# Optimization experiments

Hardware: AMD Instinct MI355X
Metric: run time of the kernel (lower is better)

## Reference

```python
import jax, jax.numpy as jnp
import numpy as np

NUM_EMBEDDINGS = 256
EMBEDDING_DIM = 8


def setup_inputs() -> dict:
    key = jax.random.key(0)
    ks = jax.random.split(key, 8)
    B, D_in, H, D_out = 1024, 512, 2048, 512
    s = lambda fan: 1.0 / np.sqrt(fan)
    return {
        "x": jax.random.normal(ks[0], (B, D_in), dtype=jnp.float32),
        "emb_W": jax.random.normal(ks[1], (NUM_EMBEDDINGS, EMBEDDING_DIM), dtype=jnp.float32),
        "W_in": jax.random.normal(ks[2], (H, D_in), dtype=jnp.float32) * s(D_in),
        "b_in": jax.random.normal(ks[3], (H,), dtype=jnp.float32) * s(D_in),
        "W_h": jax.random.normal(ks[4], (H, H), dtype=jnp.float32) * s(H),
        "b_h": jax.random.normal(ks[5], (H,), dtype=jnp.float32) * s(H),
        "W_out": jax.random.normal(ks[6], (D_out, H), dtype=jnp.float32) * s(H),
        "b_out": jax.random.normal(ks[7], (D_out,), dtype=jnp.float32) * s(H),
    }


def reference(x, emb_W, W_in, b_in, W_h, b_h, W_out, b_out):
    B, D_in = x.shape
    flat = x.reshape(-1)  # [B*D_in], row-major flatten == torch .flatten()
    # power-feature expansion: powers 1..embedding_dim stacked on axis 1
    exps = jnp.arange(1, EMBEDDING_DIM + 1, dtype=x.dtype)
    x_res = flat[:, None] ** exps[None, :]  # [B*D_in, E]
    # get_ind: NOTE source uses sum(flat_x) (not sum of squares) -- faithful
    sm = jnp.sum(x_res, axis=1, keepdims=True)              # [N,1]
    emb = jnp.sum(emb_W * emb_W, axis=1)[None, :]           # [1,K]
    dist = sm + emb - 2.0 * (x_res @ emb_W.T)               # [N,K]
    ind = jnp.argmin(dist, axis=1)                          # [N] int
    # q = ind.view_as(x.T).T : reshape to [D_in, B] then transpose
    q = ind.reshape(D_in, B).T.astype(x.dtype)              # [B, D_in]
    # straight-through: forward value q, gradient flows to x
    q = x + jax.lax.stop_gradient(q - x)
    relu = jax.nn.relu
    h = relu(q @ W_in.T + b_in)      # d_in
    for _ in range(4):               # shared d_h applied 4 times
        h = relu(h @ W_h.T + b_h)
    f = relu(h @ W_out.T + b_out)    # d_out
    q_latent_loss = jnp.float32(0.0)  # eval mode
    return (f, q_latent_loss)
```

## Files before the change

### kernel.cpp

```cpp
#include <hip/hip_runtime.h>
#include <hip/hip_bf16.h>
#include <math.h>


#define B_ROWS 1024
#define D_IN   512
#define HDIM   2048
#define NTOT   (B_ROWS * D_IN)
#define NCODE  256
#define EDIM   8

typedef __attribute__((ext_vector_type(8))) short bf16x8;
typedef __attribute__((ext_vector_type(4))) float f32x4;

__device__ inline void gload_lds16(const void* g, void* l) {
    __builtin_amdgcn_global_load_lds(
        (const __attribute__((address_space(1))) void*)g,
        (__attribute__((address_space(3))) void*)l, 16, 0, 0);
}

__device__ inline ushort bf16_hi_bits(float v, float* hi_f) {
    __hip_bfloat16 h = __float2bfloat16(v);
    *hi_f = __bfloat162float(h);
    ushort u; __builtin_memcpy(&u, &h, 2); return u;
}
__device__ inline ushort bf16_bits(float v) {
    __hip_bfloat16 h = __float2bfloat16(v);
    ushort u; __builtin_memcpy(&u, &h, 2); return u;
}

__global__ __launch_bounds__(256) void quantize_kernel(
    const float* __restrict__ x, const float* __restrict__ embW,
    ushort* __restrict__ qhi, float* __restrict__ loss_out)
{
    __shared__ float sW[NCODE][EDIM];
    __shared__ float sE[NCODE];

    const int tid = threadIdx.x;
    for (int i = tid; i < NCODE * EDIM; i += 256)
        ((float*)sW)[i] = embW[i];
    __syncthreads();
    {
        const float* w = sW[tid];
        float s0 = __fmul_rn(w[0], w[0]), s1 = __fmul_rn(w[1], w[1]);
        float s2 = __fmul_rn(w[2], w[2]), s3 = __fmul_rn(w[3], w[3]);
        float s4 = __fmul_rn(w[4], w[4]), s5 = __fmul_rn(w[5], w[5]);
        float s6 = __fmul_rn(w[6], w[6]), s7 = __fmul_rn(w[7], w[7]);
        float a = __fadd_rn(__fadd_rn(s0, s1), __fadd_rn(s2, s3));
        float b = __fadd_rn(__fadd_rn(s4, s5), __fadd_rn(s6, s7));
        sE[tid] = __fadd_rn(a, b);
    }
    __syncthreads();

    const int n = blockIdx.x * 256 + tid;
    const float v = x[n];

    float p[EDIM];
    #pragma unroll
    for (int e = 0; e < EDIM; ++e)
        p[e] = powf(v, (float)(e + 1));

    float sm;
    {
        float a = __fadd_rn(__fadd_rn(p[0], p[1]), __fadd_rn(p[2], p[3]));
        float b = __fadd_rn(__fadd_rn(p[4], p[5]), __fadd_rn(p[6], p[7]));
        sm = __fadd_rn(a, b);
    }

    float best = INFINITY;
    int bi = 0;
    for (int k = 0; k < NCODE; ++k) {
        const float4 w0 = *reinterpret_cast<const float4*>(&sW[k][0]);
        const float4 w1 = *reinterpret_cast<const float4*>(&sW[k][4]);
        float dot = 0.f;
        dot = fmaf(p[0], w0.x, dot); dot = fmaf(p[1], w0.y, dot);
        dot = fmaf(p[2], w0.z, dot); dot = fmaf(p[3], w0.w, dot);
        dot = fmaf(p[4], w1.x, dot); dot = fmaf(p[5], w1.y, dot);
        dot = fmaf(p[6], w1.z, dot); dot = fmaf(p[7], w1.w, dot);
        float d = __fsub_rn(__fadd_rn(sm, sE[k]), __fmul_rn(2.0f, dot));
        if (d < best) { best = d; bi = k; }
    }

    const int bo = n & (B_ROWS - 1);
    const int dd = n >> 10;
    qhi[bo * D_IN + dd] = bf16_bits((float)bi);

    if (blockIdx.x == 0 && tid == 0) loss_out[0] = 0.0f;
}

__global__ __launch_bounds__(256) void split_all(
    const float* __restrict__ Wi, const float* __restrict__ Wh,
    const float* __restrict__ Wo,
    ushort* __restrict__ wihi, ushort* __restrict__ wilo,
    ushort* __restrict__ whhi, ushort* __restrict__ whlo,
    ushort* __restrict__ wohi, ushort* __restrict__ wolo)
{
    const int i = blockIdx.x * 256 + threadIdx.x;
    const int R0 = HDIM * D_IN / 4;
    const int R1 = R0 + HDIM * HDIM / 4;
    const float* src; ushort* hi; ushort* lo; int j;
    if (i < R0)      { src = Wi; hi = wihi; lo = wilo; j = i; }
    else if (i < R1) { src = Wh; hi = whhi; lo = whlo; j = i - R0; }
    else             { src = Wo; hi = wohi; lo = wolo; j = i - R1; }
    float4 v = reinterpret_cast<const float4*>(src)[j];
    float f[4] = {v.x, v.y, v.z, v.w};
    ushort hh[4], ll[4];
    #pragma unroll
    for (int c = 0; c < 4; ++c) {
        float hf;
        hh[c] = bf16_hi_bits(f[c], &hf);
        ll[c] = bf16_bits(f[c] - hf);
    }
    ushort4 h = {hh[0], hh[1], hh[2], hh[3]};
    ushort4 l = {ll[0], ll[1], ll[2], ll[3]};
    reinterpret_cast<ushort4*>(hi)[j] = h;
    reinterpret_cast<ushort4*>(lo)[j] = l;
}

template<bool ALO, bool PARTIAL>
__global__ __launch_bounds__(256) void gemm_split(
    const ushort* __restrict__ Ahi, const ushort* __restrict__ Alo,
    const ushort* __restrict__ Whi, const ushort* __restrict__ Wlo,
    const float* __restrict__ bias,
    ushort* __restrict__ Ohi, ushort* __restrict__ Olo,
    float* __restrict__ OF, int N, int K, int klen)
{
    constexpr int BUF = 49152;
    constexpr int OFF_AH = 0, OFF_AL = 8192, OFF_BH = 16384;
    __shared__ char lds[2 * BUF];

    const int tid = threadIdx.x, lane = tid & 63, wid = tid >> 6;

    const int gy = gridDim.y;
    const int nwg = gridDim.x * gy;
    int lin = blockIdx.x * gy + blockIdx.y;
    int q   = nwg >> 3;
    int sw  = (lin & 7) * q + (lin >> 3);
    int bx  = sw / gy, by2 = sw % gy;
    const int bm   = (by2 & 15) << 6;
    const int kz   = by2 >> 4;
    const int kbeg = kz * klen;
    const int bn   = bx << 7;

    const int wm = (wid >> 1) << 5;
    const int wn = (wid & 1) << 6;

    constexpr int NSEGW = ALO ? 12 : 10;
    const ushort* gp[NSEGW];
    uint ldsoff[NSEGW];
    #pragma unroll
    for (int i = 0; i < NSEGW; ++i) {
        int s = wid + i * 4;
        const ushort* pl; int row0, base, sip;
        if (ALO) {
            if (s < 8)       { pl = Ahi; row0 = bm; base = OFF_AH;         sip = s; }
            else if (s < 16) { pl = Alo; row0 = bm; base = OFF_AL;         sip = s - 8; }
            else if (s < 32) { pl = Whi; row0 = bn; base = OFF_BH;         sip = s - 16; }
            else             { pl = Wlo; row0 = bn; base = OFF_BH + 16384; sip = s - 32; }
        } else {
            if (s < 8)       { pl = Ahi; row0 = bm; base = OFF_AH;         sip = s; }
            else if (s < 24) { pl = Whi; row0 = bn; base = OFF_BH;         sip = s - 8; }
            else             { pl = Wlo; row0 = bn; base = OFF_BH + 16384; sip = s - 24; }
        }
        int r  = sip * 8 + (lane >> 3);
        int ch = (lane & 7) ^ (r & 7);
        gp[i]     = pl + (size_t)(row0 + r) * K + kbeg + ch * 8;
        ldsoff[i] = base + sip * 1024;
    }

    uint aoff[2][2], boff[4][2];
    #pragma unroll
    for (int f = 0; f < 2; ++f) {
        int ar = wm + f * 16 + (lane & 15);
        #pragma unroll
        for (int s = 0; s < 2; ++s) {
            int ch = (s * 4 + (lane >> 4)) ^ (ar & 7);
            aoff[f][s] = OFF_AH + ar * 128 + ch * 16;
        }
    }
    #pragma unroll
    for (int f = 0; f < 4; ++f) {
        int br = wn + f * 16 + (lane & 15);
        #pragma unroll
        for (int s = 0; s < 2; ++s) {
            int ch = (s * 4 + (lane >> 4)) ^ (br & 7);
            boff[f][s] = OFF_BH + br * 128 + ch * 16;
        }
    }

    auto stage = [&](int kt, int b) {
        #pragma unroll
        for (int i = 0; i < NSEGW; ++i)
            gload_lds16(gp[i] + kt * 64, lds + b * BUF + ldsoff[i]);
    };

    f32x4 acc[2][4] = {};
    const int NT = klen >> 6;

    stage(0, 0);
    __syncthreads();

    for (int t = 0; t < NT; ++t) {
        const int cur = t & 1;
        if (t + 1 < NT) stage(t + 1, cur ^ 1);

        const char* lb = lds + cur * BUF;
        bf16x8 aH[2][2], aL[2][2], bH[2][4], bL[2][4];
        #pragma unroll
        for (int s = 0; s < 2; ++s) {
            #pragma unroll
            for (int f = 0; f < 2; ++f) {
                aH[s][f] = *(const bf16x8*)(lb + aoff[f][s]);
                if constexpr (ALO) aL[s][f] = *(const bf16x8*)(lb + aoff[f][s] + 8192);
            }
            #pragma unroll
            for (int f = 0; f < 4; ++f) {
                bH[s][f] = *(const bf16x8*)(lb + boff[f][s]);
                bL[s][f] = *(const bf16x8*)(lb + boff[f][s] + 16384);
            }
        }
        #pragma unroll
        for (int s = 0; s < 2; ++s) {
            #pragma unroll
            for (int fm = 0; fm < 2; ++fm)
                #pragma unroll
                for (int fn = 0; fn < 4; ++fn)
                    acc[fm][fn] = __builtin_amdgcn_mfma_f32_16x16x32_bf16(
                        aH[s][fm], bH[s][fn], acc[fm][fn], 0, 0, 0);
            #pragma unroll
            for (int fm = 0; fm < 2; ++fm)
                #pragma unroll
                for (int fn = 0; fn < 4; ++fn)
                    acc[fm][fn] = __builtin_amdgcn_mfma_f32_16x16x32_bf16(
                        aH[s][fm], bL[s][fn], acc[fm][fn], 0, 0, 0);
            if constexpr (ALO) {
                #pragma unroll
                for (int fm = 0; fm < 2; ++fm)
                    #pragma unroll
                    for (int fn = 0; fn < 4; ++fn)
                        acc[fm][fn] = __builtin_amdgcn_mfma_f32_16x16x32_bf16(
                            aL[s][fm], bH[s][fn], acc[fm][fn], 0, 0, 0);
            }
        }
        __syncthreads();
    }

    #pragma unroll
    for (int fm = 0; fm < 2; ++fm) {
        #pragma unroll
        for (int fn = 0; fn < 4; ++fn) {
            const int col = bn + wn + fn * 16 + (lane & 15);
            const int rb  = bm + wm + fm * 16 + ((lane >> 4) << 2);
            if constexpr (PARTIAL) {
                #pragma unroll
                for (int r = 0; r < 4; ++r)
                    OF[(size_t)(kz * B_ROWS + rb + r) * N + col] = acc[fm][fn][r];
            } else {
                const float bc = bias[col];
                #pragma unroll
                for (int r = 0; r < 4; ++r) {
                    float v = acc[fm][fn][r] + bc;
                    v = v > 0.f ? v : 0.f;
                    float hf;
                    ushort hb = bf16_hi_bits(v, &hf);
                    Ohi[(size_t)(rb + r) * N + col] = hb;
                    Olo[(size_t)(rb + r) * N + col] = bf16_bits(v - hf);
                }
            }
        }
    }
}

__global__ __launch_bounds__(256) void combine_relu(
    const float* __restrict__ part, const float* __restrict__ bias,
    float* __restrict__ out)
{
    const int i = blockIdx.x * 256 + threadIdx.x;
    const float4* p = (const float4*)part;
    float4 a = p[i], b = p[i + 131072], c = p[i + 262144], d = p[i + 393216];
    float4 bb = ((const float4*)bias)[i & 127];
    float4 o;
    o.x = a.x + b.x + c.x + d.x + bb.x;
    o.y = a.y + b.y + c.y + d.y + bb.y;
    o.z = a.z + b.z + c.z + d.z + bb.z;
    o.w = a.w + b.w + c.w + d.w + bb.w;
    o.x = o.x > 0.f ? o.x : 0.f;
    o.y = o.y > 0.f ? o.y : 0.f;
    o.z = o.z > 0.f ? o.z : 0.f;
    o.w = o.w > 0.f ? o.w : 0.f;
    reinterpret_cast<float4*>(out)[i] = o;
}

extern "C" void kernel_launch(void* const* d_in, const int* in_sizes, int n_in,
                              void* d_out, int out_size, void* d_ws, size_t ws_size,
                              hipStream_t stream)
{
    const float* x     = (const float*)d_in[0];
    const float* emb_W = (const float*)d_in[1];
    const float* W_in  = (const float*)d_in[2];
    const float* b_in  = (const float*)d_in[3];
    const float* W_h   = (const float*)d_in[4];
    const float* b_h   = (const float*)d_in[5];
    const float* W_out = (const float*)d_in[6];
    const float* b_out = (const float*)d_in[7];
    float* out = (float*)d_out;

    char* w = (char*)d_ws;
    const size_t MB = 1 << 20;
    ushort* qhi  = (ushort*)(w);
    ushort* h1hi = (ushort*)(w + 1*MB);
    ushort* h1lo = (ushort*)(w + 5*MB);
    ushort* h2hi = (ushort*)(w + 9*MB);
    ushort* h2lo = (ushort*)(w + 13*MB);
    float*  partial = (float*)(w + 9*MB);
    ushort* wihi = (ushort*)(w + 17*MB);
    ushort* wilo = (ushort*)(w + 19*MB);
    ushort* whhi = (ushort*)(w + 21*MB);
    ushort* whlo = (ushort*)(w + 29*MB);
    ushort* wohi = (ushort*)(w + 37*MB);
    ushort* wolo = (ushort*)(w + 39*MB);

    split_all<<<6144, 256, 0, stream>>>(W_in, W_h, W_out,
                                        wihi, wilo, whhi, whlo, wohi, wolo);

    quantize_kernel<<<NTOT / 256, 256, 0, stream>>>(x, emb_W, qhi, out + NTOT);

    gemm_split<false, false><<<dim3(16, 16), 256, 0, stream>>>(
        qhi, nullptr, wihi, wilo, b_in, h1hi, h1lo, nullptr, HDIM, D_IN, D_IN);

    ushort *shi = h1hi, *slo = h1lo, *dhi = h2hi, *dlo = h2lo;
    for (int l = 0; l < 4; ++l) {
        gemm_split<true, false><<<dim3(16, 16), 256, 0, stream>>>(
            shi, slo, whhi, whlo, b_h, dhi, dlo, nullptr, HDIM, HDIM, HDIM);
        ushort* t;
        t = shi; shi = dhi; dhi = t;
        t = slo; slo = dlo; dlo = t;
    }

    gemm_split<true, true><<<dim3(4, 64), 256, 0, stream>>>(
        shi, slo, wohi, wolo, nullptr, nullptr, nullptr, partial, D_IN, HDIM, D_IN);

    combine_relu<<<512, 256, 0, stream>>>(partial, b_out, out);
}
```

Measured before the change: 224.3 us.

## Process four elements per thread in quantize and halve GEMM K-tile to 32

The quantize kernel now handles four x elements per thread. It packs the codebook and its squared norms into one padded LDS array and folds the factor of 2 into the precomputed powers, so each codebook load from LDS is reused four times. The split-bf16 GEMM shrinks its K step from 64 to 32, which halves the LDS buffer and gives a new swizzle and load mapping, and it raises wave priority around the MFMA block. The smaller LDS footprint may allow more resident workgroups, but it doubles the number of loop iterations and barriers. Folding the 2 into the powers may change rounding slightly compared with the original distance formula.

```diff
diff --git a/kernel.cpp b/kernel.cpp
--- a/kernel.cpp
+++ b/kernel.cpp
@@ -33,58 +33,69 @@
     const float* __restrict__ x, const float* __restrict__ embW,
     ushort* __restrict__ qhi, float* __restrict__ loss_out)
 {
-    __shared__ float sW[NCODE][EDIM];
-    __shared__ float sE[NCODE];
+    __shared__ float sWE[NCODE][12];
 
     const int tid = threadIdx.x;
-    for (int i = tid; i < NCODE * EDIM; i += 256)
-        ((float*)sW)[i] = embW[i];
-    __syncthreads();
     {
-        const float* w = sW[tid];
-        float s0 = __fmul_rn(w[0], w[0]), s1 = __fmul_rn(w[1], w[1]);
-        float s2 = __fmul_rn(w[2], w[2]), s3 = __fmul_rn(w[3], w[3]);
-        float s4 = __fmul_rn(w[4], w[4]), s5 = __fmul_rn(w[5], w[5]);
-        float s6 = __fmul_rn(w[6], w[6]), s7 = __fmul_rn(w[7], w[7]);
+        const float4 a4 = *reinterpret_cast<const float4*>(&embW[tid * EDIM]);
+        const float4 b4 = *reinterpret_cast<const float4*>(&embW[tid * EDIM + 4]);
+        float s0 = __fmul_rn(a4.x, a4.x), s1 = __fmul_rn(a4.y, a4.y);
+        float s2 = __fmul_rn(a4.z, a4.z), s3 = __fmul_rn(a4.w, a4.w);
+        float s4 = __fmul_rn(b4.x, b4.x), s5 = __fmul_rn(b4.y, b4.y);
+        float s6 = __fmul_rn(b4.z, b4.z), s7 = __fmul_rn(b4.w, b4.w);
         float a = __fadd_rn(__fadd_rn(s0, s1), __fadd_rn(s2, s3));
         float b = __fadd_rn(__fadd_rn(s4, s5), __fadd_rn(s6, s7));
-        sE[tid] = __fadd_rn(a, b);
+        sWE[tid][0] = a4.x; sWE[tid][1] = a4.y; sWE[tid][2] = a4.z; sWE[tid][3] = a4.w;
+        sWE[tid][4] = b4.x; sWE[tid][5] = b4.y; sWE[tid][6] = b4.z; sWE[tid][7] = b4.w;
+        sWE[tid][8] = __fadd_rn(a, b);
     }
     __syncthreads();
 
-    const int n = blockIdx.x * 256 + tid;
-    const float v = x[n];
-
-    float p[EDIM];
-    #pragma unroll
-    for (int e = 0; e < EDIM; ++e)
-        p[e] = powf(v, (float)(e + 1));
-
-    float sm;
-    {
+    const int nbase = blockIdx.x * 1024 + tid;
+
+    float p2[4][EDIM], sm[4];
+    #pragma unroll
+    for (int j = 0; j < 4; ++j) {
+        const float v = x[nbase + j * 256];
+        float p[EDIM];
+        #pragma unroll
+        for (int e = 0; e < EDIM; ++e)
+            p[e] = powf(v, (float)(e + 1));
         float a = __fadd_rn(__fadd_rn(p[0], p[1]), __fadd_rn(p[2], p[3]));
         float b = __fadd_rn(__fadd_rn(p[4], p[5]), __fadd_rn(p[6], p[7]));
-        sm = __fadd_rn(a, b);
-    }
-
-    float best = INFINITY;
-    int bi = 0;
+        sm[j] = __fadd_rn(a, b);
+        #pragma unroll
+        for (int e = 0; e < EDIM; ++e)
+            p2[j][e] = 2.0f * p[e];
+    }
+
+    float best[4] = {INFINITY, INFINITY, INFINITY, INFINITY};
+    int   bi[4]   = {0, 0, 0, 0};
+
+    #pragma unroll 2
     for (int k = 0; k < NCODE; ++k) {
-        const float4 w0 = *reinterpret_cast<const float4*>(&sW[k][0]);
-        const float4 w1 = *reinterpret_cast<const float4*>(&sW[k][4]);
-        float dot = 0.f;
-        dot = fmaf(p[0], w0.x, dot); dot = fmaf(p[1], w0.y, dot);
-        dot = fmaf(p[2], w0.z, dot); dot = fmaf(p[3], w0.w, dot);
-        dot = fmaf(p[4], w1.x, dot); dot = fmaf(p[5], w1.y, dot);
-        dot = fmaf(p[6], w1.z, dot); dot = fmaf(p[7], w1.w, dot);
-        float d = __fsub_rn(__fadd_rn(sm, sE[k]), __fmul_rn(2.0f, dot));
-        if (d < best) { best = d; bi = k; }
-    }
-
-    const int bo = n & (B_ROWS - 1);
-    const int dd = n >> 10;
-    qhi[bo * D_IN + dd] = bf16_bits((float)bi);
-
+        const float4 w0 = *reinterpret_cast<const float4*>(&sWE[k][0]);
+        const float4 w1 = *reinterpret_cast<const float4*>(&sWE[k][4]);
+        const float  Ek = sWE[k][8];
+        #pragma unroll
+        for (int j = 0; j < 4; ++j) {
+            float dot = 0.f;
+            dot = fmaf(p2[j][0], w0.x, dot); dot = fmaf(p2[j][1], w0.y, dot);
+            dot = fmaf(p2[j][2], w0.z, dot); dot = fmaf(p2[j][3], w0.w, dot);
+            dot = fmaf(p2[j][4], w1.x, dot); dot = fmaf(p2[j][5], w1.y, dot);
+            dot = fmaf(p2[j][6], w1.z, dot); dot = fmaf(p2[j][7], w1.w, dot);
+            float d = __fsub_rn(__fadd_rn(sm[j], Ek), dot);
+            if (d < best[j]) { best[j] = d; bi[j] = k; }
+        }
+    }
+
+    #pragma unroll
+    for (int j = 0; j < 4; ++j) {
+        const int n  = nbase + j * 256;
+        const int bo = n & (B_ROWS - 1);
+        const int dd = n >> 10;
+        qhi[bo * D_IN + dd] = bf16_bits((float)bi[j]);
+    }
     if (blockIdx.x == 0 && tid == 0) loss_out[0] = 0.0f;
 }
 
@@ -125,8 +136,8 @@
     ushort* __restrict__ Ohi, ushort* __restrict__ Olo,
     float* __restrict__ OF, int N, int K, int klen)
 {
-    constexpr int BUF = 49152;
-    constexpr int OFF_AH = 0, OFF_AL = 8192, OFF_BH = 16384;
+    constexpr int BUF = 24576;
+    constexpr int OFF_AH = 0, OFF_AL = 4096, OFF_BH = 8192, OFF_BL = 16384;
     __shared__ char lds[2 * BUF];
 
     const int tid = threadIdx.x, lane = tid & 63, wid = tid >> 6;
@@ -145,7 +156,7 @@
     const int wm = (wid >> 1) << 5;
     const int wn = (wid & 1) << 6;
 
-    constexpr int NSEGW = ALO ? 12 : 10;
+    constexpr int NSEGW = ALO ? 6 : 5;
     const ushort* gp[NSEGW];
     uint ldsoff[NSEGW];
     #pragma unroll
@@ -153,49 +164,41 @@
         int s = wid + i * 4;
         const ushort* pl; int row0, base, sip;
         if (ALO) {
-            if (s < 8)       { pl = Ahi; row0 = bm; base = OFF_AH;         sip = s; }
-            else if (s < 16) { pl = Alo; row0 = bm; base = OFF_AL;         sip = s - 8; }
-            else if (s < 32) { pl = Whi; row0 = bn; base = OFF_BH;         sip = s - 16; }
-            else             { pl = Wlo; row0 = bn; base = OFF_BH + 16384; sip = s - 32; }
+            if (s < 4)       { pl = Ahi; row0 = bm; base = OFF_AH; sip = s; }
+            else if (s < 8)  { pl = Alo; row0 = bm; base = OFF_AL; sip = s - 4; }
+            else if (s < 16) { pl = Whi; row0 = bn; base = OFF_BH; sip = s - 8; }
+            else             { pl = Wlo; row0 = bn; base = OFF_BL; sip = s - 16; }
         } else {
-            if (s < 8)       { pl = Ahi; row0 = bm; base = OFF_AH;         sip = s; }
-            else if (s < 24) { pl = Whi; row0 = bn; base = OFF_BH;         sip = s - 8; }
-            else             { pl = Wlo; row0 = bn; base = OFF_BH + 16384; sip = s - 24; }
-        }
-        int r  = sip * 8 + (lane >> 3);
-        int ch = (lane & 7) ^ (r & 7);
+            if (s < 4)       { pl = Ahi; row0 = bm; base = OFF_AH; sip = s; }
+            else if (s < 12) { pl = Whi; row0 = bn; base = OFF_BH; sip = s - 4; }
+            else             { pl = Wlo; row0 = bn; base = OFF_BL; sip = s - 12; }
+        }
+        int r  = sip * 16 + (lane >> 2);
+        int ch = (lane & 3) ^ ((r >> 1) & 3);
         gp[i]     = pl + (size_t)(row0 + r) * K + kbeg + ch * 8;
         ldsoff[i] = base + sip * 1024;
     }
 
-    uint aoff[2][2], boff[4][2];
+    uint aoff[2], boff[4];
     #pragma unroll
     for (int f = 0; f < 2; ++f) {
         int ar = wm + f * 16 + (lane & 15);
-        #pragma unroll
-        for (int s = 0; s < 2; ++s) {
-            int ch = (s * 4 + (lane >> 4)) ^ (ar & 7);
-            aoff[f][s] = OFF_AH + ar * 128 + ch * 16;
-        }
+        aoff[f] = OFF_AH + ar * 64 + ((((lane >> 4)) ^ ((ar >> 1) & 3)) << 4);
     }
     #pragma unroll
     for (int f = 0; f < 4; ++f) {
         int br = wn + f * 16 + (lane & 15);
-        #pragma unroll
-        for (int s = 0; s < 2; ++s) {
-            int ch = (s * 4 + (lane >> 4)) ^ (br & 7);
-            boff[f][s] = OFF_BH + br * 128 + ch * 16;
-        }
+        boff[f] = OFF_BH + br * 64 + ((((lane >> 4)) ^ ((br >> 1) & 3)) << 4);
     }
 
     auto stage = [&](int kt, int b) {
         #pragma unroll
         for (int i = 0; i < NSEGW; ++i)
-            gload_lds16(gp[i] + kt * 64, lds + b * BUF + ldsoff[i]);
+            gload_lds16(gp[i] + kt * 32, lds + b * BUF + ldsoff[i]);
     };
 
     f32x4 acc[2][4] = {};
-    const int NT = klen >> 6;
+    const int NT = klen >> 5;
 
     stage(0, 0);
     __syncthreads();
@@ -205,43 +208,40 @@
         if (t + 1 < NT) stage(t + 1, cur ^ 1);
 
         const char* lb = lds + cur * BUF;
-        bf16x8 aH[2][2], aL[2][2], bH[2][4], bL[2][4];
-        #pragma unroll
-        for (int s = 0; s < 2; ++s) {
+        bf16x8 aH[2], aL[2], bH[4], bL[4];
+        #pragma unroll
+        for (int f = 0; f < 2; ++f) {
+            aH[f] = *(const bf16x8*)(lb + aoff[f]);
+            if constexpr (ALO) aL[f] = *(const bf16x8*)(lb + aoff[f] + 4096);
+        }
+        #pragma unroll
+        for (int f = 0; f < 4; ++f) {
+            bH[f] = *(const bf16x8*)(lb + boff[f]);
+            bL[f] = *(const bf16x8*)(lb + boff[f] + 8192);
+        }
+
+        __builtin_amdgcn_s_setprio(1);
+        #pragma unroll
+        for (int fm = 0; fm < 2; ++fm)
             #pragma unroll
-            for (int f = 0; f < 2; ++f) {
-                aH[s][f] = *(const bf16x8*)(lb + aoff[f][s]);
-                if constexpr (ALO) aL[s][f] = *(const bf16x8*)(lb + aoff[f][s] + 8192);
-            }
+            for (int fn = 0; fn < 4; ++fn)
+                acc[fm][fn] = __builtin_amdgcn_mfma_f32_16x16x32_bf16(
+                    aH[fm], bH[fn], acc[fm][fn], 0, 0, 0);
+        #pragma unroll
+        for (int fm = 0; fm < 2; ++fm)
             #pragma unroll
-            for (int f = 0; f < 4; ++f) {
-                bH[s][f] = *(const bf16x8*)(lb + boff[f][s]);
-                bL[s][f] = *(const bf16x8*)(lb + boff[f][s] + 16384);
-            }
-        }
-        #pragma unroll
-        for (int s = 0; s < 2; ++s) {
+            for (int fn = 0; fn < 4; ++fn)
+                acc[fm][fn] = __builtin_amdgcn_mfma_f32_16x16x32_bf16(
+                    aH[fm], bL[fn], acc[fm][fn], 0, 0, 0);
+        if constexpr (ALO) {
             #pragma unroll
             for (int fm = 0; fm < 2; ++fm)
                 #pragma unroll
                 for (int fn = 0; fn < 4; ++fn)
                     acc[fm][fn] = __builtin_amdgcn_mfma_f32_16x16x32_bf16(
-                        aH[s][fm], bH[s][fn], acc[fm][fn], 0, 0, 0);
-            #pragma unroll
-            for (int fm = 0; fm < 2; ++fm)
-                #pragma unroll
-                for (int fn = 0; fn < 4; ++fn)
-                    acc[fm][fn] = __builtin_amdgcn_mfma_f32_16x16x32_bf16(
-                        aH[s][fm], bL[s][fn], acc[fm][fn], 0, 0, 0);
-            if constexpr (ALO) {
-                #pragma unroll
-                for (int fm = 0; fm < 2; ++fm)
-                    #pragma unroll
-                    for (int fn = 0; fn < 4; ++fn)
-                        acc[fm][fn] = __builtin_amdgcn_mfma_f32_16x16x32_bf16(
-                            aL[s][fm], bH[s][fn], acc[fm][fn], 0, 0, 0);
-            }
-        }
+                        aL[fm], bH[fn], acc[fm][fn], 0, 0, 0);
+        }
+        __builtin_amdgcn_s_setprio(0);
         __syncthreads();
     }
 
@@ -323,7 +323,7 @@
     split_all<<<6144, 256, 0, stream>>>(W_in, W_h, W_out,
                                         wihi, wilo, whhi, whlo, wohi, wolo);
 
-    quantize_kernel<<<NTOT / 256, 256, 0, stream>>>(x, emb_W, qhi, out + NTOT);
+    quantize_kernel<<<NTOT / 1024, 256, 0, stream>>>(x, emb_W, qhi, out + NTOT);
 
     gemm_split<false, false><<<dim3(16, 16), 256, 0, stream>>>(
         qhi, nullptr, wihi, wilo, b_in, h1hi, h1lo, nullptr, HDIM, D_IN, D_IN);
```

New measurement: 274.1 us. 22.2% more time.
